# Performance work log

Hardware: AMD Instinct MI355X
Metric: run time of the kernel (lower is better)

The kernel has to match this reference:

```python
import jax, jax.numpy as jnp
import numpy as np

B, C, H, G = 4, 128, 8, 64
F = G * G  # 4096 faces on a GxG grid mesh surrogate
DH = C // H


def _build_rings():
    # BFS rings on a GxG 4-neighbor grid from face 0 (corner): ring r = {(i,j): i+j == r}
    rings_list = []
    for r in range(2 * G - 1):
        lo, hi = max(0, r - G + 1), min(r, G - 1)
        rings_list.append([i * G + (r - i) for i in range(lo, hi + 1)])
    n_rings = len(rings_list)
    max_ring = max(len(rr) for rr in rings_list)
    rings = np.full((n_rings, max_ring), -1, dtype=np.int64)
    sizes = np.zeros((n_rings,), dtype=np.int64)
    for r, rr in enumerate(rings_list):
        rings[r, :len(rr)] = rr
        sizes[r] = len(rr)
    return rings, sizes


def setup_inputs() -> dict:
    key = jax.random.key(0)
    ks = jax.random.split(key, 6)
    s = 1.0 / np.sqrt(C)
    x = jax.random.normal(ks[0], (B, C, F), dtype=jnp.float32)
    Wq0 = jax.random.normal(ks[1], (C, C), dtype=jnp.float32) * s
    Wk0 = jax.random.normal(ks[2], (C, C), dtype=jnp.float32) * s
    Wv0 = jax.random.normal(ks[3], (C, C), dtype=jnp.float32) * s
    Wq1 = jax.random.normal(ks[4], (C, C), dtype=jnp.float32) * s
    Wk1 = jax.random.normal(ks[5], (C, C), dtype=jnp.float32) * s
    rings, sizes = _build_rings()
    return {"x": x, "Wq0": Wq0, "Wk0": Wk0, "Wv0": Wv0, "Wq1": Wq1, "Wk1": Wk1,
            "rings": jnp.asarray(rings), "ring_sizes": jnp.asarray(sizes)}


def _attend(q_in, kv_in, Wq, Wk, Wv):
    # AnchorAttentionBlock, mode='resid': MHA(q=q_in, kv=kv_in) + q_in
    Bq, Cc, Nq = q_in.shape
    Nk = kv_in.shape[2]
    q = jnp.einsum('oc,bcn->bon', Wq, q_in).reshape(Bq, H, DH, Nq)
    k = jnp.einsum('oc,bcn->bon', Wk, kv_in).reshape(Bq, H, DH, Nk)
    v = jnp.einsum('oc,bcn->bon', Wv, kv_in).reshape(Bq, H, DH, Nk)
    a = jax.nn.softmax(jnp.einsum('bhdq,bhdk->bhqk', q, k) / np.float32(np.sqrt(DH)), axis=-1)
    o = jnp.einsum('bhqk,bhdk->bhdq', a, v).reshape(Bq, Cc, Nq)
    return o + q_in


def _cos_map(q_in, kv_in, Wq, Wk):
    # return_map=True, normalize=True -> per-head cosine similarity map in [-1, 1]
    Bq, _, Nq = q_in.shape
    Nk = kv_in.shape[2]
    q = jnp.einsum('oc,bcn->bon', Wq, q_in).reshape(Bq, H, DH, Nq)
    k = jnp.einsum('oc,bcn->bon', Wk, kv_in).reshape(Bq, H, DH, Nk)
    qn = q * jax.lax.rsqrt(jnp.sum(q * q, axis=2, keepdims=True) + 1e-8)
    kn = k * jax.lax.rsqrt(jnp.sum(k * k, axis=2, keepdims=True) + 1e-8)
    return jnp.einsum('bhdq,bhdk->bhqk', qn, kn)  # [B,H,Nq,Nk]


def reference(x, Wq0, Wk0, Wv0, Wq1, Wk1, rings, ring_sizes):
    rings_np = np.asarray(rings)
    sizes_np = np.asarray(ring_sizes)
    feats = x
    # Sequential BFS flood-fill: per ring, boundary faces attend over all faces.
    # Vectorized over the batch (all meshes share the grid topology + anchor).
    for r in range(rings_np.shape[0]):
        ring = rings_np[r, :int(sizes_np[r])]          # concrete face indices of this ring
        bf = feats[:, :, ring]                          # [B, C, Nb] boundary features
        bf = _attend(bf, feats, Wq0, Wk0, Wv0)          # kv = all faces (current state)
        feats = feats.at[:, :, ring].set(bf)
    anchor = int(rings_np[0, 0])
    anchor_x = feats[:, :, anchor:anchor + 1]           # [B, C, 1]
    q_x = _attend(x, anchor_x, Wq0, Wk0, Wv0)           # attention[:-1] pass on raw x
    m = _cos_map(q_x, anchor_x, Wq1, Wk1)               # [B, H, F, 1] in [-1, 1]
    final_scores = jnp.mean((m + 1.0) * 0.5, axis=1)    # [B, F, 1] in [0, 1]
    return feats, final_scores
```

## Files before the change

kernel.cpp:

```cpp
#include <hip/hip_runtime.h>
#include <hip/hip_bf16.h>

#define Bn 4
#define Cn 128
#define Fn 4096
#define NRINGS 127

typedef short bhalf4 __attribute__((ext_vector_type(4)));
typedef float f32x4  __attribute__((ext_vector_type(4)));

#define OFF_K   1048576
#define OFF_V   2097152
#define OFF_PM  3145728
#define OFF_PO  3276800
#define OFF_VA  4325376
#define OFF_KN  4325888

__device__ __forceinline__ ushort f2bf(float f) {
    __hip_bfloat16 h = __float2bfloat16(f);
    return *reinterpret_cast<ushort*>(&h);
}

__device__ __forceinline__ int ringN(int r) {
    return (r < 64 ? r : 63) - (r > 63 ? r - 63 : 0) + 1;
}

__global__ __launch_bounds__(512, 2) void initQKV(
    const float* __restrict__ x, const float* __restrict__ Wq0,
    const float* __restrict__ Wk0, const float* __restrict__ Wv0,
    ushort* __restrict__ Q0bf, ushort* __restrict__ Kbf, ushort* __restrict__ Vbf)
{
    __shared__ float xs[Cn * 64];
    __shared__ float Wls[3 * 128 * 33];
    const int wg = blockIdx.x, t = threadIdx.x;
    const int b = wg >> 6, n0 = (wg & 63) << 6;
    for (int idx = t; idx < Cn * 64; idx += 512) {
        int c = idx >> 6, j = idx & 63;
        xs[idx] = x[(size_t)((b << 7) + c) * 4096 + n0 + j];
    }
    const int o = t & 127, j0 = (t >> 7) << 4;
    float aq[16], ak[16], av[16];
#pragma unroll
    for (int k = 0; k < 16; ++k) { aq[k] = 0.f; ak[k] = 0.f; av[k] = 0.f; }
    for (int cc = 0; cc < 128; cc += 32) {
        __syncthreads();
        for (int idx = t; idx < 128 * 32; idx += 512) {
            int oo = idx >> 5, jj = idx & 31;
            Wls[oo * 33 + jj]                = Wq0[(oo << 7) + cc + jj];
            Wls[128 * 33 + oo * 33 + jj]     = Wk0[(oo << 7) + cc + jj];
            Wls[2 * 128 * 33 + oo * 33 + jj] = Wv0[(oo << 7) + cc + jj];
        }
        __syncthreads();
        for (int c2 = 0; c2 < 32; ++c2) {
            float wq = Wls[o * 33 + c2];
            float wk = Wls[128 * 33 + o * 33 + c2];
            float wv = Wls[2 * 128 * 33 + o * 33 + c2];
            const f32x4* xr4 = (const f32x4*)&xs[((cc + c2) << 6) + j0];
#pragma unroll
            for (int k4 = 0; k4 < 4; ++k4) {
                f32x4 xv = xr4[k4];
#pragma unroll
                for (int e = 0; e < 4; ++e) {
                    int k = (k4 << 2) + e;
                    aq[k] += wq * xv[e]; ak[k] += wk * xv[e]; av[k] += wv * xv[e];
                }
            }
        }
    }
    const int h = o >> 4, d = o & 15;
    const int bh = (b << 3) + h;
#pragma unroll
    for (int k = 0; k < 16; ++k) {
        int col = n0 + j0 + k;
        size_t qi = (size_t)(bh * 4096 + col) * 16 + d;
        Q0bf[qi] = f2bf(aq[k]);
        Kbf[qi]  = f2bf(ak[k]);
    }
    uint vv[8];
#pragma unroll
    for (int k2 = 0; k2 < 8; ++k2)
        vv[k2] = (uint)f2bf(av[2*k2]) | ((uint)f2bf(av[2*k2+1]) << 16);
    uint4* dst = (uint4*)&Vbf[(size_t)(bh * 16 + d) * 4096 + n0 + j0];
    dst[0] = make_uint4(vv[0], vv[1], vv[2], vv[3]);
    dst[1] = make_uint4(vv[4], vv[5], vv[6], vv[7]);
}

template<bool TAIL>
__global__ __launch_bounds__(512, 2) void fusedRing(
    const float* __restrict__ x, const float* __restrict__ Wk0,
    const float* __restrict__ Wv0, const ushort* __restrict__ Q0bf,
    ushort* __restrict__ Kbf, ushort* __restrict__ Vbf,
    float2* __restrict__ pml, float* __restrict__ po,
    float* __restrict__ feats, int r)
{
    __shared__ ushort Kls[512 * 24];
    __shared__ ushort Vls[16 * 520];
    __shared__ ushort Qls[64 * 24];
    __shared__ float  outc[12 * 128];

    const int t = threadIdx.x, wgid = blockIdx.x;
    const int b = wgid >> 6, h = (wgid >> 3) & 7, sp = wgid & 7;
    const int bh = (b << 3) + h;
    const int keybase = sp << 9;

    const int n   = TAIL ? 0 : ringN(r);
    const int rp  = r - 1;
    const int np  = (r > 0) ? ringN(rp) : 0;
    const int i0p = (r > 0) ? (rp > 63 ? rp - 63 : 0) : 0;

    int jlo = 0, cnt = 0;
    if (r > 0) {
        int A = keybase - rp;
        int mlo = (A > 0) ? (A + 62) / 63 : 0;
        int mhiN = keybase + 511 - rp;
        int mhi = (mhiN < 0) ? -1 : mhiN / 63;
        int jl = mlo - i0p;      if (jl < 0) jl = 0;
        int jh = mhi - i0p;      if (jh > np - 1) jh = np - 1;
        jlo = jl;
        cnt = (jh >= jl) ? (jh - jl + 1) : 0;
    }

    uint4 k0q, k1q, v0q, v1q, qreg;
    if (!TAIL) {
        const uint4* ks = (const uint4*)(Kbf + (size_t)((bh << 12) + keybase + t) * 16);
        k0q = ks[0]; k1q = ks[1];
        int vdd = t >> 5, vcc = t & 31;
        const uint4* vs = (const uint4*)(Vbf + (size_t)(bh * 16 + vdd) * 4096
                                         + keybase + (vcc << 4));
        v0q = vs[0]; v1q = vs[1];
        if (t < 128) {
            int q = t >> 1, half = t & 1;
            int i0F = (r > 63) ? r - 63 : 0;
            int cq = (q < n) ? (63 * (i0F + q) + r) : 0;
            qreg = *(const uint4*)(Q0bf + (size_t)((bh << 12) + cq) * 16 + half * 8);
        }
    }

    if (r > 0 && cnt > 0) {
        const int bufp = rp & 1;
        const int slot = t >> 7, c = t & 127;
        const int hh = c >> 4, dd = c & 15;
        const int p0b = ((bufp << 5) + (b << 3) + hh) * 1024;
#pragma unroll
        for (int base = 0; base < 12; base += 4) {
            int ow = base + slot;
            if (ow < cnt) {
                int j = jlo + ow;
                int col = 63 * (i0p + j) + rp;
                int p0 = p0b + j;
                float2 ml[16];
                float mstar = -1e30f;
#pragma unroll
                for (int s2 = 0; s2 < 16; ++s2) {
                    ml[s2] = pml[p0 + (s2 << 6)];
                    mstar = fmaxf(mstar, ml[s2].x);
                }
                float lstar = 0.f, osum = 0.f;
#pragma unroll
                for (int s2 = 0; s2 < 16; ++s2) {
                    float e = __expf(ml[s2].x - mstar);
                    lstar += ml[s2].y * e;
                    osum  += po[(p0 + (s2 << 6)) * 16 + dd] * e;
                }
                float outv = osum / lstar + x[(size_t)((b << 7) + c) * 4096 + col];
                outc[ow * 128 + c] = outv;
                if (h == 0) feats[(size_t)((b << 7) + c) * 4096 + col] = outv;
            }
        }
    }
    if (TAIL) return;

    {
        *(uint4*)&Kls[t * 24]     = k0q;
        *(uint4*)&Kls[t * 24 + 8] = k1q;
        int vdd = t >> 5, vcc = t & 31;
        *(uint4*)&Vls[vdd * 520 + (vcc << 4)]     = v0q;
        *(uint4*)&Vls[vdd * 520 + (vcc << 4) + 8] = v1q;
        if (t < 128) {
            int q = t >> 1, half = t & 1;
            *(uint4*)&Qls[q * 24 + half * 8] = qreg;
        }
    }
    __syncthreads();

    if (cnt > 0) {
        int slot = t >> 5, task = t & 31;
        if (slot < cnt) {
            int j = jlo + slot;
            int col = 63 * (i0p + j) + rp;
            int isV = task >> 4, dd = task & 15;
            int row = (h << 4) + dd;
            const float* W = isV ? Wv0 : Wk0;
            const float* oc = &outc[slot * 128];
            float acc = 0.f;
            for (int c2 = 0; c2 < Cn; ++c2)
                acc += W[(row << 7) + c2] * oc[c2];
            ushort bfv = f2bf(acc);
            if (isV) {
                Vbf[(size_t)(bh * 16 + dd) * 4096 + col] = bfv;
                Vls[dd * 520 + (col - keybase)] = bfv;
            } else {
                Kbf[(size_t)((bh << 12) + col) * 16 + dd] = bfv;
                Kls[(col - keybase) * 24 + dd] = bfv;
            }
        }
    }
    __syncthreads();

    const int w = t >> 6, lane = t & 63;
    const int qt = w & 3, kh = w >> 2;
    const int buf = r & 1;
    if (qt * 16 < n) {
        const int lm = lane & 15, lg = lane >> 4;
        bhalf4 qf = *(const bhalf4*)&Qls[(qt * 16 + lm) * 24 + (lg << 2)];
        const int key0 = kh << 8;
        f32x4 sc[16];
#pragma unroll
        for (int kt = 0; kt < 16; ++kt) {
            bhalf4 kf = *(const bhalf4*)&Kls[(key0 + (kt << 4) + lm) * 24 + (lg << 2)];
            f32x4 z = {0.f, 0.f, 0.f, 0.f};
            sc[kt] = __builtin_amdgcn_mfma_f32_16x16x16bf16_1k(kf, qf, z, 0, 0, 0);
        }
        float m = -1e30f;
#pragma unroll
        for (int kt = 0; kt < 16; ++kt)
            m = fmaxf(m, fmaxf(fmaxf(sc[kt][0], sc[kt][1]), fmaxf(sc[kt][2], sc[kt][3])));
        m = fmaxf(m, __shfl_xor(m, 16));
        m = fmaxf(m, __shfl_xor(m, 32));
        float lsum = 0.f;
        f32x4 oacc = {0.f, 0.f, 0.f, 0.f};
#pragma unroll
        for (int kt = 0; kt < 16; ++kt) {
            float p0 = __expf((sc[kt][0] - m) * 0.25f);
            float p1 = __expf((sc[kt][1] - m) * 0.25f);
            float p2 = __expf((sc[kt][2] - m) * 0.25f);
            float p3 = __expf((sc[kt][3] - m) * 0.25f);
            lsum += (p0 + p1) + (p2 + p3);
            bhalf4 pv;
            pv[0] = (short)f2bf(p0); pv[1] = (short)f2bf(p1);
            pv[2] = (short)f2bf(p2); pv[3] = (short)f2bf(p3);
            bhalf4 vf = *(const bhalf4*)&Vls[lm * 520 + key0 + (kt << 4) + (lg << 2)];
            oacc = __builtin_amdgcn_mfma_f32_16x16x16bf16_1k(pv, vf, oacc, 0, 0, 0);
        }
        lsum += __shfl_xor(lsum, 16);
        lsum += __shfl_xor(lsum, 32);
        const int pb = ((((buf << 5) + bh) << 4) | ((sp << 1) + kh)) * 64;
        if (lg == 0)
            pml[pb + qt * 16 + lm] = make_float2(m * 0.25f, lsum);
#pragma unroll
        for (int reg = 0; reg < 4; ++reg)
            po[(pb + qt * 16 + (lg << 2) + reg) * 16 + lm] = oacc[reg];
    }
}

__global__ __launch_bounds__(128) void epi1(
    const float* __restrict__ feats, const float* __restrict__ Wv0,
    const float* __restrict__ Wk1, const int* __restrict__ rings,
    float* __restrict__ Va, float* __restrict__ Kn)
{
    int b = blockIdx.x;
    int i = threadIdx.x;
    int anchor = rings[0];
    __shared__ float la[128];
    __shared__ float kk2[128];
    la[i] = feats[(size_t)((b << 7) + i) * 4096 + anchor];
    __syncthreads();
    float va = 0.f, k1 = 0.f;
    for (int c = 0; c < 128; ++c) {
        va += Wv0[i * 128 + c] * la[c];
        k1 += Wk1[i * 128 + c] * la[c];
    }
    Va[b * 128 + i] = va;
    kk2[i] = k1 * k1;
    __syncthreads();
    float ss = 0.f;
    int hb = i & ~15;
    for (int d = 0; d < 16; ++d) ss += kk2[hb + d];
    Kn[b * 128 + i] = k1 * rsqrtf(ss + 1e-8f);
}

__global__ __launch_bounds__(256) void epi2(
    const float* __restrict__ x, const float* __restrict__ Wq1,
    const float* __restrict__ Va, const float* __restrict__ Kn,
    float* __restrict__ scores)
{
    __shared__ float Wt[128 * 132];
    __shared__ float lxT[128 * 36];
    const int bid = blockIdx.x, t = threadIdx.x;
    const int b = bid >> 7, col0 = (bid & 127) << 5;
    for (int idx = t; idx < 128 * 128; idx += 256) {
        int o = idx >> 7, c = idx & 127;
        Wt[c*132 + o] = Wq1[idx];
    }
    for (int idx = t; idx < 128 * 32; idx += 256) {
        int c = idx >> 5, col = idx & 31;
        lxT[c*36 + col] = x[(size_t)((b << 7) + c) * 4096 + col0 + col] + Va[(b << 7) + c];
    }
    __syncthreads();
    const int og = t & 31, colg = t >> 5;
    const int o0 = og << 2, cl0 = colg << 2;
    float acc[4][4];
#pragma unroll
    for (int i = 0; i < 4; ++i)
#pragma unroll
        for (int j = 0; j < 4; ++j) acc[i][j] = 0.f;
    for (int c = 0; c < 128; ++c) {
        f32x4 wv = *(const f32x4*)&Wt[c*132 + o0];
        f32x4 xv = *(const f32x4*)&lxT[c*36 + cl0];
#pragma unroll
        for (int i = 0; i < 4; ++i)
#pragma unroll
            for (int j = 0; j < 4; ++j) acc[i][j] += wv[i] * xv[j];
    }
    float kn4[4];
#pragma unroll
    for (int i = 0; i < 4; ++i) kn4[i] = Kn[(b << 7) + o0 + i];
    float res[4];
#pragma unroll
    for (int j = 0; j < 4; ++j) {
        float ss = acc[0][j]*acc[0][j] + acc[1][j]*acc[1][j]
                 + acc[2][j]*acc[2][j] + acc[3][j]*acc[3][j];
        ss += __shfl_xor(ss, 1);
        ss += __shfl_xor(ss, 2);
        float rs = rsqrtf(ss + 1e-8f);
        float mp = (acc[0][j]*kn4[0] + acc[1][j]*kn4[1]
                  + acc[2][j]*kn4[2] + acc[3][j]*kn4[3]) * rs;
#pragma unroll
        for (int msk = 1; msk <= 16; msk <<= 1) mp += __shfl_xor(mp, msk);
        res[j] = 0.5f + mp * (1.0f / 16.0f);
    }
    if (og == 0) {
#pragma unroll
        for (int j = 0; j < 4; ++j)
            scores[(b << 12) + col0 + cl0 + j] = res[j];
    }
}

extern "C" void kernel_launch(void* const* d_in, const int* in_sizes, int n_in,
                              void* d_out, int out_size, void* d_ws, size_t ws_size,
                              hipStream_t stream) {
    const float* x   = (const float*)d_in[0];
    const float* Wq0 = (const float*)d_in[1];
    const float* Wk0 = (const float*)d_in[2];
    const float* Wv0 = (const float*)d_in[3];
    const float* Wq1 = (const float*)d_in[4];
    const float* Wk1 = (const float*)d_in[5];
    const int*   rings = (const int*)d_in[6];

    float* feats  = (float*)d_out;
    float* scores = feats + Bn * Cn * Fn;

    float*  ws   = (float*)d_ws;
    ushort* Q0bf = (ushort*)ws;
    ushort* Kbf  = (ushort*)(ws + OFF_K);
    ushort* Vbf  = (ushort*)(ws + OFF_V);
    float2* pml  = (float2*)(ws + OFF_PM);
    float*  po   = ws + OFF_PO;
    float*  Va   = ws + OFF_VA;
    float*  Kn   = ws + OFF_KN;

    initQKV<<<256, 512, 0, stream>>>(x, Wq0, Wk0, Wv0, Q0bf, Kbf, Vbf);

    for (int r = 0; r < NRINGS; ++r) {
        fusedRing<false><<<256, 512, 0, stream>>>(
            x, Wk0, Wv0, Q0bf, Kbf, Vbf, pml, po, feats, r);
    }
    fusedRing<true><<<256, 512, 0, stream>>>(
        x, Wk0, Wv0, Q0bf, Kbf, Vbf, pml, po, feats, NRINGS);

    epi1<<<Bn, 128, 0, stream>>>(feats, Wv0, Wk1, rings, Va, Kn);
    epi2<<<512, 256, 0, stream>>>(x, Wq1, Va, Kn, scores);
}
```

Baseline: 1.638 ms.

## Issue QK score MFMAs before K/V recompute and patch updated keys afterward

Moves the Q·K MFMA score computation ahead of the barrier that waits for the freshly recomputed K/V columns, so the matrix work overlaps the scalar K/V projection. The few keys rewritten in this ring (up to 9) are then patched in the score registers with a scalar dot product plus cross-lane shuffles. This adds register pressure (16 f32x4 live across the projection loop) and unrolled patching branches, and it depends on the patched score exactly matching the MFMA layout.

```diff
diff --git a/kernel.cpp b/kernel.cpp
--- a/kernel.cpp
+++ b/kernel.cpp
@@ -20,7 +20,9 @@
     __hip_bfloat16 h = __float2bfloat16(f);
     return *reinterpret_cast<ushort*>(&h);
 }
-
+__device__ __forceinline__ float bfbits2f(short s) {
+    return __uint_as_float(((uint)(ushort)s) << 16);
+}
 __device__ __forceinline__ int ringN(int r) {
     return (r < 64 ? r : 63) - (r > 63 ? r - 63 : 0) + 1;
 }
@@ -182,6 +184,24 @@
         }
     }
     __syncthreads();
+
+    const int w = t >> 6, lane = t & 63;
+    const int qt = w & 3, kh = w >> 2;
+    const int buf = r & 1;
+    const int lm = lane & 15, lg = lane >> 4;
+    const bool wact = (qt * 16 < n);
+    const int key0 = kh << 8;
+    bhalf4 qf;
+    f32x4 sc[16];
+    if (wact) {
+        qf = *(const bhalf4*)&Qls[(qt * 16 + lm) * 24 + (lg << 2)];
+#pragma unroll
+        for (int kt = 0; kt < 16; ++kt) {
+            bhalf4 kf = *(const bhalf4*)&Kls[(key0 + (kt << 4) + lm) * 24 + (lg << 2)];
+            f32x4 z = {0.f, 0.f, 0.f, 0.f};
+            sc[kt] = __builtin_amdgcn_mfma_f32_16x16x16bf16_1k(kf, qf, z, 0, 0, 0);
+        }
+    }
 
     if (cnt > 0) {
         int slot = t >> 5, task = t & 31;
@@ -207,19 +227,37 @@
     }
     __syncthreads();
 
-    const int w = t >> 6, lane = t & 63;
-    const int qt = w & 3, kh = w >> 2;
-    const int buf = r & 1;
-    if (qt * 16 < n) {
-        const int lm = lane & 15, lg = lane >> 4;
-        bhalf4 qf = *(const bhalf4*)&Qls[(qt * 16 + lm) * 24 + (lg << 2)];
-        const int key0 = kh << 8;
-        f32x4 sc[16];
-#pragma unroll
-        for (int kt = 0; kt < 16; ++kt) {
-            bhalf4 kf = *(const bhalf4*)&Kls[(key0 + (kt << 4) + lm) * 24 + (lg << 2)];
-            f32x4 z = {0.f, 0.f, 0.f, 0.f};
-            sc[kt] = __builtin_amdgcn_mfma_f32_16x16x16bf16_1k(kf, qf, z, 0, 0, 0);
+    if (wact) {
+        if (cnt > 0) {
+#pragma unroll
+            for (int ci = 0; ci < 9; ++ci) {
+                if (ci < cnt) {
+                    int col = 63 * (i0p + jlo + ci) + rp;
+                    int k = col - keybase;
+                    if ((k >> 8) == kh) {
+                        bhalf4 kf2 = *(const bhalf4*)&Kls[k * 24 + (lg << 2)];
+                        float part = bfbits2f(qf[0]) * bfbits2f(kf2[0])
+                                   + bfbits2f(qf[1]) * bfbits2f(kf2[1])
+                                   + bfbits2f(qf[2]) * bfbits2f(kf2[2])
+                                   + bfbits2f(qf[3]) * bfbits2f(kf2[3]);
+                        part += __shfl_xor(part, 16);
+                        part += __shfl_xor(part, 32);
+                        int kt0 = (k & 255) >> 4;
+                        int pos = k & 15;
+                        int lgs = pos >> 2, es = pos & 3;
+#pragma unroll
+                        for (int kt = 0; kt < 16; ++kt) {
+                            if (kt == kt0) {
+#pragma unroll
+                                for (int e = 0; e < 4; ++e) {
+                                    if (e == es && lg == lgs)
+                                        sc[kt][e] = part;
+                                }
+                            }
+                        }
+                    }
+                }
+            }
         }
         float m = -1e30f;
 #pragma unroll
```

Result: slower. 1.802 ms (+10.1%).
